# Kernel tuning notes

Hardware: AMD Instinct MI355X
Metric: run time of the kernel (lower is better)

Reference implementation:

```python
import jax, jax.numpy as jnp
import numpy as np

N_EDGES = 1048576
N_CENTERS = 32768
N_SPECIES = 4
L_MAX = 3
N_BASIS = 12
N_MAX = 8
R_CUT = 5.0
NORM = 1.0 / np.sqrt(32.0)  # hypers['normalize'] = avg_num_neighbors = 32
SH_SPLITS = [0, 1, 4, 9, 16]  # cumulative offsets of (2l+1)


def real_sph_harm_lmax3(u):
    # u: [E,3] unit vectors; returns [E,16] real normalized spherical harmonics (sphericart order m=-l..l)
    x, y, z = u[:, 0], u[:, 1], u[:, 2]
    c0 = 0.5 * np.sqrt(1.0 / np.pi)
    c1 = np.sqrt(3.0 / (4.0 * np.pi))
    x2, y2, z2 = x * x, y * y, z * z
    sh = [
        jnp.full_like(x, c0),
        c1 * y, c1 * z, c1 * x,
        0.5 * np.sqrt(15.0 / np.pi) * x * y,
        0.5 * np.sqrt(15.0 / np.pi) * y * z,
        0.25 * np.sqrt(5.0 / np.pi) * (3.0 * z2 - 1.0),
        0.5 * np.sqrt(15.0 / np.pi) * x * z,
        0.25 * np.sqrt(15.0 / np.pi) * (x2 - y2),
        0.25 * np.sqrt(35.0 / (2.0 * np.pi)) * y * (3.0 * x2 - y2),
        0.5 * np.sqrt(105.0 / np.pi) * x * y * z,
        0.25 * np.sqrt(21.0 / (2.0 * np.pi)) * y * (5.0 * z2 - 1.0),
        0.25 * np.sqrt(7.0 / np.pi) * (5.0 * z2 * z - 3.0 * z),
        0.25 * np.sqrt(21.0 / (2.0 * np.pi)) * x * (5.0 * z2 - 1.0),
        0.25 * np.sqrt(105.0 / np.pi) * z * (x2 - y2),
        0.25 * np.sqrt(35.0 / (2.0 * np.pi)) * x * (x2 - y2),
    ]
    return jnp.stack(sh, axis=1)


def setup_inputs() -> dict:
    key = jax.random.key(0)
    k1, k2, k3, k4 = jax.random.split(key, 4)
    vectors = jax.random.normal(k1, (N_EDGES, 3), dtype=jnp.float32) * 1.5
    radial_weights = jax.random.normal(k2, (L_MAX + 1, N_BASIS, N_MAX), dtype=jnp.float32) * 0.1
    center_index = jax.random.randint(k3, (N_EDGES,), 0, N_CENTERS, dtype=jnp.int64)
    neighbor_species_index = jax.random.randint(k4, (N_EDGES,), 0, N_SPECIES, dtype=jnp.int64)
    return {"vectors": vectors, "radial_weights": radial_weights,
            "center_index": center_index, "neighbor_species_index": neighbor_species_index}


def reference(vectors, radial_weights, center_index, neighbor_species_index):
    # distances and unit vectors
    r = jnp.sqrt(jnp.sum(vectors * vectors, axis=-1) + 1e-12)  # [E]
    u = vectors / r[:, None]
    # smooth radial basis phi_n(r) = sin((n+1) pi r / r_cut)/r, normalized (LE-like)
    ns = jnp.arange(1, N_BASIS + 1, dtype=vectors.dtype)
    phi = jnp.sin(np.pi / R_CUT * r[:, None] * ns[None, :]) / r[:, None] * NORM  # [E, N_BASIS]
    sh = real_sph_harm_lmax3(u)  # [E,16]
    # scatter target: (center, neighbor_species) channel
    idx = center_index * N_SPECIES + neighbor_species_index  # [E]
    densities = []
    for l in range(L_MAX + 1):
        m_l = 2 * l + 1
        sh_l = jax.lax.slice_in_dim(sh, SH_SPLITS[l], SH_SPLITS[l + 1], axis=1)  # [E, 2l+1]
        rad_l = phi @ radial_weights[l]  # [E, N_MAX]
        edge_l = rad_l[:, None, :] * sh_l[:, :, None]  # [E, 2l+1, N_MAX] outer product
        dens = jax.ops.segment_sum(edge_l.reshape(edge_l.shape[0], -1), idx,
                                   num_segments=N_CENTERS * N_SPECIES)  # [N*S, m*n]
        dens = dens.reshape(N_CENTERS, N_SPECIES, m_l, N_MAX)
        dens = jnp.transpose(dens, (0, 2, 1, 3)).reshape(N_CENTERS, m_l, N_SPECIES * N_MAX)
        densities.append(dens)  # c^{a_i l}_{Ai, m, a_j n}
    # concatenate the per-l TensorMap blocks along the m axis -> [N, sum(2l+1), S*N_MAX]
    return jnp.concatenate(densities, axis=1)
```

## Files before the change

### kernel.cpp

```cpp
#include <hip/hip_runtime.h>
#include <math.h>

#define N_EDGES     1048576
#define NBKT        4096
#define SEG_PER_BKT 32
#define N_BASIS     12
#define CAP         384
#define HBLK        256
#define HEPB        (N_EDGES / HBLK)


#define WS_BLKHIST  0
#define WS_TOTALS   (HBLK * NBKT * 4)
#define WS_OFFSETS  (WS_TOTALS + NBKT * 4)
#define WS_REC      (WS_OFFSETS + NBKT * 4)
#define WS_NEED     (WS_REC + (size_t)N_EDGES * 4)

__device__ __forceinline__ void compute_edge(float x, float y, float z,
                                             float* __restrict__ ph,
                                             float* __restrict__ sh)
{
    const float r2    = fmaf(x, x, fmaf(y, y, z * z)) + 1e-12f;
    const float inv_r = rsqrtf(r2);
    const float r     = r2 * inv_r;
    x *= inv_r; y *= inv_r; z *= inv_r;

    const float t = 0.6283185307179586f * r;
    float s1, c1;
    __sincosf(t, &s1, &c1);
    const float twoc = 2.0f * c1;
    const float scale = 0.17677669529663687f * inv_r;
    float skm1 = 0.0f, sk = s1;
    #pragma unroll
    for (int b = 0; b < N_BASIS; ++b) {
        ph[b] = sk * scale;
        const float nxt = fmaf(twoc, sk, -skm1);
        skm1 = sk; sk = nxt;
    }

    const float x2 = x * x, y2 = y * y, z2 = z * z;
    sh[0]  = 0.28209479177387814f;
    sh[1]  = 0.4886025119029199f * y;
    sh[2]  = 0.4886025119029199f * z;
    sh[3]  = 0.4886025119029199f * x;
    sh[4]  = 1.0925484305920792f * x * y;
    sh[5]  = 1.0925484305920792f * y * z;
    sh[6]  = 0.31539156525252005f * (3.0f * z2 - 1.0f);
    sh[7]  = 1.0925484305920792f * x * z;
    sh[8]  = 0.5462742152960396f * (x2 - y2);
    sh[9]  = 0.5900435899266435f * y * (3.0f * x2 - y2);
    sh[10] = 2.890611442640554f  * x * y * z;
    sh[11] = 0.4570457994644658f * y * (5.0f * z2 - 1.0f);
    sh[12] = 0.3731763325901154f * (5.0f * z2 * z - 3.0f * z);
    sh[13] = 0.4570457994644658f * x * (5.0f * z2 - 1.0f);
    sh[14] = 1.445305721320277f  * z * (x2 - y2);
    sh[15] = 0.5900435899266435f * x * (x2 - y2);
}

__global__ __launch_bounds__(256) void hist_kernel(
    const int* __restrict__ cidx, const int* __restrict__ sidx,
    int* __restrict__ blkhist)
{
    __shared__ int h[NBKT];
    const int t = threadIdx.x;
    #pragma unroll
    for (int i = t; i < NBKT; i += 256) h[i] = 0;
    __syncthreads();
    const int base = blockIdx.x * HEPB;
    #pragma unroll
    for (int k = 0; k < HEPB / 256; ++k) {
        const int e = base + k * 256 + t;
        const int seg = (cidx[e] << 2) | sidx[e];
        atomicAdd(&h[seg >> 5], 1);
    }
    __syncthreads();
    #pragma unroll
    for (int i = t; i < NBKT; i += 256)
        blkhist[blockIdx.x * NBKT + i] = h[i];
}

__global__ __launch_bounds__(128) void scanA_kernel(
    int* __restrict__ blkhist, int* __restrict__ totals)
{
    const int bkt = blockIdx.x * 128 + threadIdx.x;
    int run = 0;
    for (int blk = 0; blk < HBLK; ++blk) {
        const int v = blkhist[blk * NBKT + bkt];
        blkhist[blk * NBKT + bkt] = run;
        run += v;
    }
    totals[bkt] = run;
}

__global__ __launch_bounds__(1024) void scanB_kernel(
    const int* __restrict__ totals, int* __restrict__ offsets)
{
    __shared__ int tmp[1024];
    const int t = threadIdx.x;
    const int4 tv = ((const int4*)totals)[t];
    const int a0 = tv.x, a1 = a0 + tv.y, a2 = a1 + tv.z, a3 = a2 + tv.w;
    tmp[t] = a3;
    __syncthreads();
    #pragma unroll
    for (int d = 1; d < 1024; d <<= 1) {
        const int v = (t >= d) ? tmp[t - d] : 0;
        __syncthreads();
        tmp[t] += v;
        __syncthreads();
    }
    const int ex = tmp[t] - a3;
    offsets[4 * t + 0] = ex;
    offsets[4 * t + 1] = ex + a0;
    offsets[4 * t + 2] = ex + a1;
    offsets[4 * t + 3] = ex + a2;
}

__global__ __launch_bounds__(256) void partition_kernel(
    const int* __restrict__ cidx, const int* __restrict__ sidx,
    const int* __restrict__ blkhist, const int* __restrict__ offsets,
    unsigned int* __restrict__ records)
{
    __shared__ int bb[NBKT];
    __shared__ int lcnt[NBKT];
    const int t = threadIdx.x;
    #pragma unroll
    for (int i = t; i < NBKT; i += 256) {
        bb[i] = offsets[i] + blkhist[blockIdx.x * NBKT + i];
        lcnt[i] = 0;
    }
    __syncthreads();
    const int base = blockIdx.x * HEPB;
    #pragma unroll
    for (int k = 0; k < HEPB / 256; ++k) {
        const int e = base + k * 256 + t;
        const int seg = (cidx[e] << 2) | sidx[e];
        const int bkt = seg >> 5;
        const int r = atomicAdd(&lcnt[bkt], 1);
        records[bb[bkt] + r] = ((unsigned)(seg & 31) << 20) | (unsigned)e;
    }
}

__global__ __launch_bounds__(256) void compute_kernel(
    const unsigned int* __restrict__ records,
    const int* __restrict__ offsets, const int* __restrict__ counts,
    const float* __restrict__ vectors,
    const float* __restrict__ rw,
    float* __restrict__ out)
{
    __shared__ float4 pay[CAP * 7];
    __shared__ int shist[SEG_PER_BKT];
    __shared__ int soff[SEG_PER_BKT + 1];
    __shared__ int scur[SEG_PER_BKT];

    const int t = threadIdx.x;
    const int b = blockIdx.x;
    const int n = t & 7;
    const int g = t >> 3;

    const int off = offsets[b];
    const int cnt = counts[b];

    if (cnt > CAP) {
        float Wn[4][N_BASIS];
        #pragma unroll
        for (int l = 0; l < 4; ++l)
            #pragma unroll
            for (int bb2 = 0; bb2 < N_BASIS; ++bb2)
                Wn[l][bb2] = rw[(l * N_BASIS + bb2) * 8 + n];
        float acc[16];
        #pragma unroll
        for (int L = 0; L < 16; ++L) acc[L] = 0.0f;
        for (int j = 0; j < cnt; ++j) {
            const unsigned rec = records[off + j];
            if ((int)(rec >> 20) != g) continue;
            const int eid = rec & 0xFFFFF;
            float ph[N_BASIS], sh[16];
            compute_edge(vectors[3*eid], vectors[3*eid+1], vectors[3*eid+2], ph, sh);
            float rad[4];
            #pragma unroll
            for (int l = 0; l < 4; ++l) {
                float a = 0.0f;
                #pragma unroll
                for (int bb2 = 0; bb2 < N_BASIS; ++bb2)
                    a = fmaf(ph[bb2], Wn[l][bb2], a);
                rad[l] = a;
            }
            #pragma unroll
            for (int L = 0; L < 16; ++L) {
                const int l = (L == 0) ? 0 : (L < 4) ? 1 : (L < 9) ? 2 : 3;
                acc[L] = fmaf(sh[L], rad[l], acc[L]);
            }
        }
        const int seg = b * SEG_PER_BKT + g;
        float* op = out + (size_t)(seg >> 2) * 512 + (seg & 3) * 8 + n;
        #pragma unroll
        for (int L = 0; L < 16; ++L) op[L * 32] = acc[L];
        return;
    }

    if (t < SEG_PER_BKT) shist[t] = 0;
    __syncthreads();

    unsigned recs[2];
    const int iters = (cnt + 255) >> 8;
    #pragma unroll
    for (int it = 0; it < 2; ++it) {
        const int i = it * 256 + t;
        if (it < iters && i < cnt) {
            recs[it] = records[off + i];
            atomicAdd(&shist[recs[it] >> 20], 1);
        }
    }
    __syncthreads();

    if (t < SEG_PER_BKT) {
        const int h = shist[t];
        int v = h;
        #pragma unroll
        for (int d = 1; d < 32; d <<= 1) {
            const int u = __shfl_up(v, d, 32);
            if (t >= d) v += u;
        }
        soff[t] = v - h;
        scur[t] = v - h;
        if (t == 31) soff[32] = v;
    }
    __syncthreads();

    #pragma unroll
    for (int it = 0; it < 2; ++it) {
        const int i = it * 256 + t;
        if (it < iters && i < cnt) {
            const int sl  = recs[it] >> 20;
            const int eid = recs[it] & 0xFFFFF;
            const float x = vectors[3 * eid + 0];
            const float y = vectors[3 * eid + 1];
            const float z = vectors[3 * eid + 2];
            const int r = atomicAdd(&scur[sl], 1);
            float ph[N_BASIS], sh[16];
            compute_edge(x, y, z, ph, sh);
            float4* pp = &pay[r * 7];
            pp[0] = make_float4(ph[0], ph[1], ph[2], ph[3]);
            pp[1] = make_float4(ph[4], ph[5], ph[6], ph[7]);
            pp[2] = make_float4(ph[8], ph[9], ph[10], ph[11]);
            pp[3] = make_float4(sh[0], sh[1], sh[2], sh[3]);
            pp[4] = make_float4(sh[4], sh[5], sh[6], sh[7]);
            pp[5] = make_float4(sh[8], sh[9], sh[10], sh[11]);
            pp[6] = make_float4(sh[12], sh[13], sh[14], sh[15]);
        }
    }
    __syncthreads();

    float Wn[4][N_BASIS];
    #pragma unroll
    for (int l = 0; l < 4; ++l)
        #pragma unroll
        for (int bb2 = 0; bb2 < N_BASIS; ++bb2)
            Wn[l][bb2] = rw[(l * N_BASIS + bb2) * 8 + n];

    const int js = soff[g];
    const int je = soff[g + 1];

    float acc[16];
    #pragma unroll
    for (int L = 0; L < 16; ++L) acc[L] = 0.0f;

    for (int j = js; j < je; ++j) {
        const float4* pp = &pay[j * 7];
        const float4 p0 = pp[0], p1 = pp[1], p2 = pp[2];
        const float4 s0 = pp[3], s1 = pp[4], s2 = pp[5], s3 = pp[6];

        float rad[4];
        #pragma unroll
        for (int l = 0; l < 4; ++l) {
            float a =      p0.x * Wn[l][0];
            a = fmaf(p0.y, Wn[l][1],  a);
            a = fmaf(p0.z, Wn[l][2],  a);
            a = fmaf(p0.w, Wn[l][3],  a);
            a = fmaf(p1.x, Wn[l][4],  a);
            a = fmaf(p1.y, Wn[l][5],  a);
            a = fmaf(p1.z, Wn[l][6],  a);
            a = fmaf(p1.w, Wn[l][7],  a);
            a = fmaf(p2.x, Wn[l][8],  a);
            a = fmaf(p2.y, Wn[l][9],  a);
            a = fmaf(p2.z, Wn[l][10], a);
            a = fmaf(p2.w, Wn[l][11], a);
            rad[l] = a;
        }
        acc[0]  = fmaf(s0.x, rad[0], acc[0]);
        acc[1]  = fmaf(s0.y, rad[1], acc[1]);
        acc[2]  = fmaf(s0.z, rad[1], acc[2]);
        acc[3]  = fmaf(s0.w, rad[1], acc[3]);
        acc[4]  = fmaf(s1.x, rad[2], acc[4]);
        acc[5]  = fmaf(s1.y, rad[2], acc[5]);
        acc[6]  = fmaf(s1.z, rad[2], acc[6]);
        acc[7]  = fmaf(s1.w, rad[2], acc[7]);
        acc[8]  = fmaf(s2.x, rad[2], acc[8]);
        acc[9]  = fmaf(s2.y, rad[3], acc[9]);
        acc[10] = fmaf(s2.z, rad[3], acc[10]);
        acc[11] = fmaf(s2.w, rad[3], acc[11]);
        acc[12] = fmaf(s3.x, rad[3], acc[12]);
        acc[13] = fmaf(s3.y, rad[3], acc[13]);
        acc[14] = fmaf(s3.z, rad[3], acc[14]);
        acc[15] = fmaf(s3.w, rad[3], acc[15]);
    }

    const int seg = b * SEG_PER_BKT + g;
    float* op = out + (size_t)(seg >> 2) * 512 + (seg & 3) * 8 + n;
    #pragma unroll
    for (int L = 0; L < 16; ++L) op[L * 32] = acc[L];
}

__global__ __launch_bounds__(256) void atomic_kernel(
    const float* __restrict__ vectors, const float* __restrict__ rw,
    const int* __restrict__ cidx, const int* __restrict__ sidx,
    float* __restrict__ out)
{
    const int e = blockIdx.x * 256 + threadIdx.x;
    if (e >= N_EDGES) return;
    float ph[N_BASIS], sh[16];
    compute_edge(vectors[3*e], vectors[3*e+1], vectors[3*e+2], ph, sh);
    float* op = out + (size_t)cidx[e] * 512 + sidx[e] * 8;
    for (int l = 0; l < 4; ++l) {
        const int L0 = l * l;
        const int ml = 2 * l + 1;
        for (int nn = 0; nn < 8; ++nn) {
            float rad = 0.0f;
            for (int bb2 = 0; bb2 < N_BASIS; ++bb2)
                rad = fmaf(ph[bb2], rw[(l * N_BASIS + bb2) * 8 + nn], rad);
            for (int mm = 0; mm < ml; ++mm)
                atomicAdd(op + (L0 + mm) * 32 + nn, sh[L0 + mm] * rad);
        }
    }
}

extern "C" void kernel_launch(void* const* d_in, const int* in_sizes, int n_in,
                              void* d_out, int out_size, void* d_ws, size_t ws_size,
                              hipStream_t stream) {
    const float* vectors = (const float*)d_in[0];
    const float* rw      = (const float*)d_in[1];
    const int*   cidx    = (const int*)d_in[2];
    const int*   sidx    = (const int*)d_in[3];
    float*       out     = (float*)d_out;

    if (ws_size < (size_t)WS_NEED) {
        hipMemsetAsync(out, 0, (size_t)out_size * sizeof(float), stream);
        hipLaunchKernelGGL(atomic_kernel, dim3(N_EDGES / 256), dim3(256), 0, stream,
                           vectors, rw, cidx, sidx, out);
        return;
    }

    char* ws = (char*)d_ws;
    int*          blkhist = (int*)(ws + WS_BLKHIST);
    int*          totals  = (int*)(ws + WS_TOTALS);
    int*          offsets = (int*)(ws + WS_OFFSETS);
    unsigned int* records = (unsigned int*)(ws + WS_REC);

    hipLaunchKernelGGL(hist_kernel,      dim3(HBLK),     dim3(256),  0, stream, cidx, sidx, blkhist);
    hipLaunchKernelGGL(scanA_kernel,     dim3(NBKT/128), dim3(128),  0, stream, blkhist, totals);
    hipLaunchKernelGGL(scanB_kernel,     dim3(1),        dim3(1024), 0, stream, totals, offsets);
    hipLaunchKernelGGL(partition_kernel, dim3(HBLK),     dim3(256),  0, stream, cidx, sidx, blkhist, offsets, records);
    hipLaunchKernelGGL(compute_kernel,   dim3(NBKT),     dim3(256),  0, stream, records, offsets, totals, vectors, rw, out);
}
```

Baseline: 153.6 us.

## Store unit vectors instead of harmonics in LDS and balance segment-to-group assignment

The compute kernel now stores only the radial basis and the unit vector per edge in shared memory (5 float4 instead of 7), and recomputes the spherical harmonics inside the per-segment accumulation loop. It also ranks segments by edge count and maps the thread groups so that heavy segments land on low group indices, which should cut wavefront divergence from uneven segment lengths. The cost is that each of the 8 threads in a group recomputes the harmonics for every edge, adding ALU work in the hot loop in exchange for less LDS traffic and occupancy pressure.

```diff
diff --git a/kernel.cpp b/kernel.cpp
--- a/kernel.cpp
+++ b/kernel.cpp
@@ -16,14 +16,14 @@
 #define WS_REC      (WS_OFFSETS + NBKT * 4)
 #define WS_NEED     (WS_REC + (size_t)N_EDGES * 4)
 
-__device__ __forceinline__ void compute_edge(float x, float y, float z,
-                                             float* __restrict__ ph,
-                                             float* __restrict__ sh)
+__device__ __forceinline__ void compute_ph(float x, float y, float z,
+                                           float* __restrict__ ph,
+                                           float& ux, float& uy, float& uz)
 {
     const float r2    = fmaf(x, x, fmaf(y, y, z * z)) + 1e-12f;
     const float inv_r = rsqrtf(r2);
     const float r     = r2 * inv_r;
-    x *= inv_r; y *= inv_r; z *= inv_r;
+    ux = x * inv_r; uy = y * inv_r; uz = z * inv_r;
 
     const float t = 0.6283185307179586f * r;
     float s1, c1;
@@ -37,7 +37,11 @@
         const float nxt = fmaf(twoc, sk, -skm1);
         skm1 = sk; sk = nxt;
     }
-
+}
+
+__device__ __forceinline__ void compute_sh(float x, float y, float z,
+                                           float* __restrict__ sh)
+{
     const float x2 = x * x, y2 = y * y, z2 = z * z;
     sh[0]  = 0.28209479177387814f;
     sh[1]  = 0.4886025119029199f * y;
@@ -57,6 +61,15 @@
     sh[15] = 0.5900435899266435f * x * (x2 - y2);
 }
 
+__device__ __forceinline__ void compute_edge(float x, float y, float z,
+                                             float* __restrict__ ph,
+                                             float* __restrict__ sh)
+{
+    float ux, uy, uz;
+    compute_ph(x, y, z, ph, ux, uy, uz);
+    compute_sh(ux, uy, uz, sh);
+}
+
 __global__ __launch_bounds__(256) void hist_kernel(
     const int* __restrict__ cidx, const int* __restrict__ sidx,
     int* __restrict__ blkhist)
@@ -147,10 +160,11 @@
     const float* __restrict__ rw,
     float* __restrict__ out)
 {
-    __shared__ float4 pay[CAP * 7];
+    __shared__ float4 pay[CAP * 5];
     __shared__ int shist[SEG_PER_BKT];
     __shared__ int soff[SEG_PER_BKT + 1];
     __shared__ int scur[SEG_PER_BKT];
+    __shared__ int inv_s[SEG_PER_BKT];
 
     const int t = threadIdx.x;
     const int b = blockIdx.x;
@@ -224,6 +238,13 @@
         soff[t] = v - h;
         scur[t] = v - h;
         if (t == 31) soff[32] = v;
+        int rank = 0;
+        #pragma unroll 8
+        for (int d = 0; d < SEG_PER_BKT; ++d) {
+            const int cd = __shfl(h, d, 32);
+            rank += (cd > h) || (cd == h && d < t);
+        }
+        inv_s[rank] = t;
     }
     __syncthreads();
 
@@ -237,16 +258,14 @@
             const float y = vectors[3 * eid + 1];
             const float z = vectors[3 * eid + 2];
             const int r = atomicAdd(&scur[sl], 1);
-            float ph[N_BASIS], sh[16];
-            compute_edge(x, y, z, ph, sh);
-            float4* pp = &pay[r * 7];
+            float ph[N_BASIS];
+            float ux, uy, uz;
+            compute_ph(x, y, z, ph, ux, uy, uz);
+            float4* pp = &pay[r * 5];
             pp[0] = make_float4(ph[0], ph[1], ph[2], ph[3]);
             pp[1] = make_float4(ph[4], ph[5], ph[6], ph[7]);
             pp[2] = make_float4(ph[8], ph[9], ph[10], ph[11]);
-            pp[3] = make_float4(sh[0], sh[1], sh[2], sh[3]);
-            pp[4] = make_float4(sh[4], sh[5], sh[6], sh[7]);
-            pp[5] = make_float4(sh[8], sh[9], sh[10], sh[11]);
-            pp[6] = make_float4(sh[12], sh[13], sh[14], sh[15]);
+            pp[3] = make_float4(ux, uy, uz, 0.0f);
         }
     }
     __syncthreads();
@@ -258,17 +277,17 @@
         for (int bb2 = 0; bb2 < N_BASIS; ++bb2)
             Wn[l][bb2] = rw[(l * N_BASIS + bb2) * 8 + n];
 
-    const int js = soff[g];
-    const int je = soff[g + 1];
+    const int myseg = inv_s[g];
+    const int js = soff[myseg];
+    const int je = js + shist[myseg];
 
     float acc[16];
     #pragma unroll
     for (int L = 0; L < 16; ++L) acc[L] = 0.0f;
 
     for (int j = js; j < je; ++j) {
-        const float4* pp = &pay[j * 7];
-        const float4 p0 = pp[0], p1 = pp[1], p2 = pp[2];
-        const float4 s0 = pp[3], s1 = pp[4], s2 = pp[5], s3 = pp[6];
+        const float4* pp = &pay[j * 5];
+        const float4 p0 = pp[0], p1 = pp[1], p2 = pp[2], u = pp[3];
 
         float rad[4];
         #pragma unroll
@@ -287,25 +306,28 @@
             a = fmaf(p2.w, Wn[l][11], a);
             rad[l] = a;
         }
-        acc[0]  = fmaf(s0.x, rad[0], acc[0]);
-        acc[1]  = fmaf(s0.y, rad[1], acc[1]);
-        acc[2]  = fmaf(s0.z, rad[1], acc[2]);
-        acc[3]  = fmaf(s0.w, rad[1], acc[3]);
-        acc[4]  = fmaf(s1.x, rad[2], acc[4]);
-        acc[5]  = fmaf(s1.y, rad[2], acc[5]);
-        acc[6]  = fmaf(s1.z, rad[2], acc[6]);
-        acc[7]  = fmaf(s1.w, rad[2], acc[7]);
-        acc[8]  = fmaf(s2.x, rad[2], acc[8]);
-        acc[9]  = fmaf(s2.y, rad[3], acc[9]);
-        acc[10] = fmaf(s2.z, rad[3], acc[10]);
-        acc[11] = fmaf(s2.w, rad[3], acc[11]);
-        acc[12] = fmaf(s3.x, rad[3], acc[12]);
-        acc[13] = fmaf(s3.y, rad[3], acc[13]);
-        acc[14] = fmaf(s3.z, rad[3], acc[14]);
-        acc[15] = fmaf(s3.w, rad[3], acc[15]);
-    }
-
-    const int seg = b * SEG_PER_BKT + g;
+
+        const float xx = u.x, yy = u.y, zz = u.z;
+        const float x2 = xx * xx, y2 = yy * yy, z2 = zz * zz;
+        acc[0]  = fmaf(0.28209479177387814f,                 rad[0], acc[0]);
+        acc[1]  = fmaf(0.4886025119029199f * yy,             rad[1], acc[1]);
+        acc[2]  = fmaf(0.4886025119029199f * zz,             rad[1], acc[2]);
+        acc[3]  = fmaf(0.4886025119029199f * xx,             rad[1], acc[3]);
+        acc[4]  = fmaf(1.0925484305920792f * xx * yy,        rad[2], acc[4]);
+        acc[5]  = fmaf(1.0925484305920792f * yy * zz,        rad[2], acc[5]);
+        acc[6]  = fmaf(0.31539156525252005f * (3.0f*z2-1.0f),rad[2], acc[6]);
+        acc[7]  = fmaf(1.0925484305920792f * xx * zz,        rad[2], acc[7]);
+        acc[8]  = fmaf(0.5462742152960396f * (x2 - y2),      rad[2], acc[8]);
+        acc[9]  = fmaf(0.5900435899266435f * yy * (3.0f*x2-y2), rad[3], acc[9]);
+        acc[10] = fmaf(2.890611442640554f  * xx * yy * zz,   rad[3], acc[10]);
+        acc[11] = fmaf(0.4570457994644658f * yy * (5.0f*z2-1.0f), rad[3], acc[11]);
+        acc[12] = fmaf(0.3731763325901154f * (5.0f*z2*zz-3.0f*zz), rad[3], acc[12]);
+        acc[13] = fmaf(0.4570457994644658f * xx * (5.0f*z2-1.0f), rad[3], acc[13]);
+        acc[14] = fmaf(1.445305721320277f  * zz * (x2 - y2), rad[3], acc[14]);
+        acc[15] = fmaf(0.5900435899266435f * xx * (x2 - y2), rad[3], acc[15]);
+    }
+
+    const int seg = b * SEG_PER_BKT + myseg;
     float* op = out + (size_t)(seg >> 2) * 512 + (seg & 3) * 8 + n;
     #pragma unroll
     for (int L = 0; L < 16; ++L) op[L * 32] = acc[L];
```

After: 156.6 us. Within noise of the previous version (+1.9%).

## Replace histogram/scan/partition pipeline with fixed-capacity atomic bucket scatter plus overflow list

Applied to the files above, without the earlier changes.

Removes the three-stage histogram, two-level scan and partition kernels and instead scatters each edge record into a fixed-capacity per-bucket slot using a padded global atomic cursor. Records beyond the capacity go to a global overflow list that the compute kernel scans linearly in its slow path. This cuts kernel launches and the passes over the large per-block histogram, at the cost of contended global atomics and a serial overflow scan if any bucket exceeds capacity. A redundant duplicate shared-memory store was also added.

```diff
diff --git a/kernel.cpp b/kernel.cpp
--- a/kernel.cpp
+++ b/kernel.cpp
@@ -5,16 +5,16 @@
 #define NBKT        4096
 #define SEG_PER_BKT 32
 #define N_BASIS     12
-#define CAP         384
-#define HBLK        256
-#define HEPB        (N_EDGES / HBLK)
-
-
-#define WS_BLKHIST  0
-#define WS_TOTALS   (HBLK * NBKT * 4)
-#define WS_OFFSETS  (WS_TOTALS + NBKT * 4)
-#define WS_REC      (WS_OFFSETS + NBKT * 4)
-#define WS_NEED     (WS_REC + (size_t)N_EDGES * 4)
+#define CAP         344
+#define CSTRIDE     16
+#define OVF_CAP     65536
+
+
+#define WS_CURSORS  0
+#define WS_OVFCNT   (NBKT * CSTRIDE * 4)
+#define WS_OVF      (WS_OVFCNT + 64)
+#define WS_REC      (WS_OVF + OVF_CAP * 8)
+#define WS_NEED     (WS_REC + (size_t)NBKT * CAP * 4)
 
 __device__ __forceinline__ void compute_edge(float x, float y, float z,
                                              float* __restrict__ ph,
@@ -57,92 +57,27 @@
     sh[15] = 0.5900435899266435f * x * (x2 - y2);
 }
 
-__global__ __launch_bounds__(256) void hist_kernel(
+__global__ __launch_bounds__(256) void scatter_kernel(
     const int* __restrict__ cidx, const int* __restrict__ sidx,
-    int* __restrict__ blkhist)
+    int* __restrict__ cursors, int* __restrict__ ovf_cnt,
+    uint2* __restrict__ ovf, unsigned int* __restrict__ records)
 {
-    __shared__ int h[NBKT];
-    const int t = threadIdx.x;
-    #pragma unroll
-    for (int i = t; i < NBKT; i += 256) h[i] = 0;
-    __syncthreads();
-    const int base = blockIdx.x * HEPB;
-    #pragma unroll
-    for (int k = 0; k < HEPB / 256; ++k) {
-        const int e = base + k * 256 + t;
-        const int seg = (cidx[e] << 2) | sidx[e];
-        atomicAdd(&h[seg >> 5], 1);
-    }
-    __syncthreads();
-    #pragma unroll
-    for (int i = t; i < NBKT; i += 256)
-        blkhist[blockIdx.x * NBKT + i] = h[i];
-}
-
-__global__ __launch_bounds__(128) void scanA_kernel(
-    int* __restrict__ blkhist, int* __restrict__ totals)
-{
-    const int bkt = blockIdx.x * 128 + threadIdx.x;
-    int run = 0;
-    for (int blk = 0; blk < HBLK; ++blk) {
-        const int v = blkhist[blk * NBKT + bkt];
-        blkhist[blk * NBKT + bkt] = run;
-        run += v;
-    }
-    totals[bkt] = run;
-}
-
-__global__ __launch_bounds__(1024) void scanB_kernel(
-    const int* __restrict__ totals, int* __restrict__ offsets)
-{
-    __shared__ int tmp[1024];
-    const int t = threadIdx.x;
-    const int4 tv = ((const int4*)totals)[t];
-    const int a0 = tv.x, a1 = a0 + tv.y, a2 = a1 + tv.z, a3 = a2 + tv.w;
-    tmp[t] = a3;
-    __syncthreads();
-    #pragma unroll
-    for (int d = 1; d < 1024; d <<= 1) {
-        const int v = (t >= d) ? tmp[t - d] : 0;
-        __syncthreads();
-        tmp[t] += v;
-        __syncthreads();
-    }
-    const int ex = tmp[t] - a3;
-    offsets[4 * t + 0] = ex;
-    offsets[4 * t + 1] = ex + a0;
-    offsets[4 * t + 2] = ex + a1;
-    offsets[4 * t + 3] = ex + a2;
-}
-
-__global__ __launch_bounds__(256) void partition_kernel(
-    const int* __restrict__ cidx, const int* __restrict__ sidx,
-    const int* __restrict__ blkhist, const int* __restrict__ offsets,
-    unsigned int* __restrict__ records)
-{
-    __shared__ int bb[NBKT];
-    __shared__ int lcnt[NBKT];
-    const int t = threadIdx.x;
-    #pragma unroll
-    for (int i = t; i < NBKT; i += 256) {
-        bb[i] = offsets[i] + blkhist[blockIdx.x * NBKT + i];
-        lcnt[i] = 0;
-    }
-    __syncthreads();
-    const int base = blockIdx.x * HEPB;
-    #pragma unroll
-    for (int k = 0; k < HEPB / 256; ++k) {
-        const int e = base + k * 256 + t;
-        const int seg = (cidx[e] << 2) | sidx[e];
-        const int bkt = seg >> 5;
-        const int r = atomicAdd(&lcnt[bkt], 1);
-        records[bb[bkt] + r] = ((unsigned)(seg & 31) << 20) | (unsigned)e;
+    const int e = blockIdx.x * 256 + threadIdx.x;
+    const int seg = (cidx[e] << 2) | sidx[e];
+    const int bkt = seg >> 5;
+    const int pos = atomicAdd(&cursors[bkt * CSTRIDE], 1);
+    if (pos < CAP) {
+        records[bkt * CAP + pos] = ((unsigned)(seg & 31) << 20) | (unsigned)e;
+    } else {
+        const int o = atomicAdd(ovf_cnt, 1);
+        if (o < OVF_CAP) ovf[o] = make_uint2((unsigned)seg, (unsigned)e);
     }
 }
 
 __global__ __launch_bounds__(256) void compute_kernel(
     const unsigned int* __restrict__ records,
-    const int* __restrict__ offsets, const int* __restrict__ counts,
+    const int* __restrict__ cursors,
+    const int* __restrict__ ovf_cnt, const uint2* __restrict__ ovf,
     const float* __restrict__ vectors,
     const float* __restrict__ rw,
     float* __restrict__ out)
@@ -157,8 +92,8 @@
     const int n = t & 7;
     const int g = t >> 3;
 
-    const int off = offsets[b];
-    const int cnt = counts[b];
+    const int off = b * CAP;
+    const int cnt = cursors[b * CSTRIDE];
 
     if (cnt > CAP) {
         float Wn[4][N_BASIS];
@@ -170,10 +105,33 @@
         float acc[16];
         #pragma unroll
         for (int L = 0; L < 16; ++L) acc[L] = 0.0f;
-        for (int j = 0; j < cnt; ++j) {
+
+        for (int j = 0; j < CAP; ++j) {
             const unsigned rec = records[off + j];
             if ((int)(rec >> 20) != g) continue;
             const int eid = rec & 0xFFFFF;
+            float ph[N_BASIS], sh[16];
+            compute_edge(vectors[3*eid], vectors[3*eid+1], vectors[3*eid+2], ph, sh);
+            float rad[4];
+            #pragma unroll
+            for (int l = 0; l < 4; ++l) {
+                float a = 0.0f;
+                #pragma unroll
+                for (int bb2 = 0; bb2 < N_BASIS; ++bb2)
+                    a = fmaf(ph[bb2], Wn[l][bb2], a);
+                rad[l] = a;
+            }
+            #pragma unroll
+            for (int L = 0; L < 16; ++L) {
+                const int l = (L == 0) ? 0 : (L < 4) ? 1 : (L < 9) ? 2 : 3;
+                acc[L] = fmaf(sh[L], rad[l], acc[L]);
+            }
+        }
+        const int m = (*ovf_cnt < OVF_CAP) ? *ovf_cnt : OVF_CAP;
+        for (int i = 0; i < m; ++i) {
+            const uint2 oe = ovf[i];
+            if ((int)(oe.x >> 5) != b || (int)(oe.x & 31) != g) continue;
+            const int eid = (int)oe.y;
             float ph[N_BASIS], sh[16];
             compute_edge(vectors[3*eid], vectors[3*eid+1], vectors[3*eid+2], ph, sh);
             float rad[4];
@@ -245,6 +203,7 @@
             pp[2] = make_float4(ph[8], ph[9], ph[10], ph[11]);
             pp[3] = make_float4(sh[0], sh[1], sh[2], sh[3]);
             pp[4] = make_float4(sh[4], sh[5], sh[6], sh[7]);
+            pp[5] = make_float4(sh[8], sh[9], sh[11 - 2], sh[11]);
             pp[5] = make_float4(sh[8], sh[9], sh[10], sh[11]);
             pp[6] = make_float4(sh[12], sh[13], sh[14], sh[15]);
         }
@@ -351,14 +310,15 @@
     }
 
     char* ws = (char*)d_ws;
-    int*          blkhist = (int*)(ws + WS_BLKHIST);
-    int*          totals  = (int*)(ws + WS_TOTALS);
-    int*          offsets = (int*)(ws + WS_OFFSETS);
+    int*          cursors = (int*)(ws + WS_CURSORS);
+    int*          ovfcnt  = (int*)(ws + WS_OVFCNT);
+    uint2*        ovf     = (uint2*)(ws + WS_OVF);
     unsigned int* records = (unsigned int*)(ws + WS_REC);
 
-    hipLaunchKernelGGL(hist_kernel,      dim3(HBLK),     dim3(256),  0, stream, cidx, sidx, blkhist);
-    hipLaunchKernelGGL(scanA_kernel,     dim3(NBKT/128), dim3(128),  0, stream, blkhist, totals);
-    hipLaunchKernelGGL(scanB_kernel,     dim3(1),        dim3(1024), 0, stream, totals, offsets);
-    hipLaunchKernelGGL(partition_kernel, dim3(HBLK),     dim3(256),  0, stream, cidx, sidx, blkhist, offsets, records);
-    hipLaunchKernelGGL(compute_kernel,   dim3(NBKT),     dim3(256),  0, stream, records, offsets, totals, vectors, rw, out);
-}
+    hipMemsetAsync(ws, 0, WS_OVFCNT + 64, stream);
+
+    hipLaunchKernelGGL(scatter_kernel, dim3(N_EDGES / 256), dim3(256), 0, stream,
+                       cidx, sidx, cursors, ovfcnt, ovf, records);
+    hipLaunchKernelGGL(compute_kernel, dim3(NBKT), dim3(256), 0, stream,
+                       records, cursors, ovfcnt, ovf, vectors, rw, out);
+}
```

After: 176.3 us. 14.7% more time.
